# Kernel tuning notes

Hardware: AMD Instinct MI355X
Metric: run time of the kernel (lower is better)

Reference implementation:

```python
import jax, jax.numpy as jnp
import numpy as np

ALPHA = 1.702
LIMIT = 7.0
TOP_K = 4


def setup_inputs() -> dict:
    key = jax.random.key(0)
    ks = jax.random.split(key, 7)
    B, S, H, E, I = 2, 1024, 1024, 16, 2048
    scale_w = 1.0 / np.sqrt(H)
    return {
        "hidden_states": jax.random.normal(ks[0], (B, S, H), jnp.float32),
        "router_weight": jax.random.normal(ks[1], (E, H), jnp.float32) * scale_w,
        "router_bias": jax.random.normal(ks[2], (E,), jnp.float32) * 0.01,
        "gate_up_proj": jax.random.normal(ks[3], (E, H, 2 * I), jnp.float32) * scale_w,
        "gate_up_proj_bias": jax.random.normal(ks[4], (E, 2 * I), jnp.float32) * 0.01,
        "down_proj": jax.random.normal(ks[5], (E, I, H), jnp.float32) * (1.0 / np.sqrt(I)),
        "down_proj_bias": jax.random.normal(ks[6], (E, H), jnp.float32) * 0.01,
    }


def reference(hidden_states, router_weight, router_bias, gate_up_proj,
              gate_up_proj_bias, down_proj, down_proj_bias):
    B, S, H = hidden_states.shape
    E = router_weight.shape[0]
    dt = hidden_states.dtype

    # Router: linear -> softmax -> top-k -> renormalize
    router_logits = jnp.einsum('bsh,eh->bse', hidden_states, router_weight) + router_bias
    router_probs = jax.nn.softmax(router_logits, axis=-1)
    topk_weights, topk_indices = jax.lax.top_k(router_probs, TOP_K)  # [B,S,K]
    topk_weights = topk_weights / jnp.sum(topk_weights, axis=-1, keepdims=True)

    # Sparsity mask [B,S,E]: 1 for active experts (semantics of tt.sparse_matmul)
    onehot = jax.nn.one_hot(topk_indices, E, dtype=dt)        # [B,S,K,E]
    sparsity = jnp.sum(onehot, axis=2)                         # [B,S,E] (0/1)

    # Fused gate+up projection (interleaved layout), masked per-expert
    gate_up = jnp.einsum('bsh,ehf->bsef', hidden_states, gate_up_proj)  # [B,S,E,2I]
    gate_up = gate_up * sparsity[..., None]
    gate = gate_up[..., 0::2] + gate_up_proj_bias[:, 0::2]     # [B,S,E,I]
    up = gate_up[..., 1::2] + gate_up_proj_bias[:, 1::2]

    gate = jnp.minimum(gate, LIMIT)
    up = jnp.clip(up, -LIMIT, LIMIT)
    glu = gate * jax.nn.sigmoid(gate * ALPHA)
    activated = (up + 1.0) * glu                               # [B,S,E,I]

    # Down projection, masked per-expert, then bias
    down = jnp.einsum('bsei,eih->bseh', activated, down_proj)  # [B,S,E,H]
    down = down * sparsity[..., None] + down_proj_bias         # bias broadcasts [E,H]

    # Scatter top-k weights to full expert dim and combine
    full_weights = jnp.sum(onehot * topk_weights[..., None], axis=2)   # [B,S,E]
    output = jnp.sum(down * full_weights[..., None], axis=2)           # [B,S,H]
    return output, topk_weights
```

## Files before the change

kernel.cpp:

```cpp
#include <hip/hip_runtime.h>

#define TOKENS 2048
#define HD 1024
#define NEXP 16
#define TWO_I 4096
#define ID 2048

typedef short short8 __attribute__((ext_vector_type(8)));
typedef float f32x4 __attribute__((ext_vector_type(4)));
typedef unsigned short ushort;

static __device__ __forceinline__ ushort f2bf(float f) {
    union { float f; unsigned u; } v; v.f = f;
    unsigned r = v.u + 0x7FFFu + ((v.u >> 16) & 1u);
    return (ushort)(r >> 16);
}

static __device__ __forceinline__ void gload_lds16(const void* g, void* l) {
    __builtin_amdgcn_global_load_lds(
        (const __attribute__((address_space(1))) unsigned int*)(g),
        (__attribute__((address_space(3))) unsigned int*)(l), 16, 0, 0);
}

__global__ __launch_bounds__(256) void cvt_kernel(const float* __restrict__ hs,
                                                  ushort* __restrict__ hb) {
    int i = (blockIdx.x * 256 + threadIdx.x) * 4;
    float4 v = *(const float4*)(hs + i);
    union { ushort b[4]; float2 f2; } u;
    u.b[0] = f2bf(v.x); u.b[1] = f2bf(v.y); u.b[2] = f2bf(v.z); u.b[3] = f2bf(v.w);
    *(float2*)(hb + i) = u.f2;
}

__global__ __launch_bounds__(256) void transpose_cvt_kernel(
    const float* __restrict__ src, ushort* __restrict__ dst, int K, int N) {
    const int e = blockIdx.z;
    const int n0 = blockIdx.x * 64;
    const int k0 = blockIdx.y * 64;
    __shared__ float T[64][68];
    const float* s = src + (size_t)e * K * N + (size_t)k0 * N + n0;
    const int r = threadIdx.x >> 4;
    const int c4 = (threadIdx.x & 15) * 4;
#pragma unroll
    for (int i = 0; i < 64; i += 16) {
        float4 v = *(const float4*)(s + (size_t)(r + i) * N + c4);
        T[r + i][c4 + 0] = v.x; T[r + i][c4 + 1] = v.y;
        T[r + i][c4 + 2] = v.z; T[r + i][c4 + 3] = v.w;
    }
    __syncthreads();
    const int n = threadIdx.x >> 2;
    const int kc = (threadIdx.x & 3) * 16;
    union { ushort b[16]; short8 v[2]; } o;
#pragma unroll
    for (int j = 0; j < 16; ++j) o.b[j] = f2bf(T[kc + j][n]);
    ushort* d = dst + (size_t)e * N * K + (size_t)(n0 + n) * K + k0 + kc;
    *(short8*)(d) = o.v[0];
    *(short8*)(d + 8) = o.v[1];
}

__global__ __launch_bounds__(256) void router_kernel(
    const float* __restrict__ hs, const float* __restrict__ rw,
    const float* __restrict__ rb, float* __restrict__ topk_w_out,
    int* __restrict__ topk_idx, int* __restrict__ counts) {
    const int wave = threadIdx.x >> 6;
    const int lane = threadIdx.x & 63;
    const int t = blockIdx.x * 4 + wave;

    float h[16];
#pragma unroll
    for (int j = 0; j < 16; ++j) h[j] = hs[t * HD + j * 64 + lane];

    __shared__ float lg[4][NEXP];
#pragma unroll
    for (int e = 0; e < NEXP; ++e) {
        float acc = 0.f;
#pragma unroll
        for (int j = 0; j < 16; ++j) acc += h[j] * rw[e * HD + j * 64 + lane];
#pragma unroll
        for (int s = 32; s > 0; s >>= 1) acc += __shfl_xor(acc, s);
        if (lane == 0) lg[wave][e] = acc + rb[e];
    }
    if (lane == 0) {
        float mx = lg[wave][0];
        for (int e = 1; e < NEXP; ++e) mx = fmaxf(mx, lg[wave][e]);
        float pr[NEXP];
        for (int e = 0; e < NEXP; ++e) pr[e] = __expf(lg[wave][e] - mx);
        int idx[4]; float wv[4]; float sum4 = 0.f;
        for (int k = 0; k < 4; ++k) {
            int bi = 0; float bv = -1.f;
            for (int e = 0; e < NEXP; ++e)
                if (pr[e] > bv) { bv = pr[e]; bi = e; }
            idx[k] = bi; wv[k] = bv; pr[bi] = -2.f; sum4 += bv;
        }
        for (int k = 0; k < 4; ++k) {
            topk_w_out[t * 4 + k] = wv[k] / sum4;
            topk_idx[t * 4 + k] = idx[k];
            atomicAdd(&counts[idx[k]], 1);
        }
    }
}

__global__ void scan_kernel(const int* __restrict__ counts, int* __restrict__ offsets,
                            int* __restrict__ cursor) {
    if (threadIdx.x == 0 && blockIdx.x == 0) {
        int o = 0;
        for (int e = 0; e < NEXP; ++e) { offsets[e] = o; cursor[e] = o; o += counts[e]; }
        offsets[NEXP] = o;
    }
}

__global__ __launch_bounds__(256) void build_kernel(
    const int* __restrict__ topk_idx, const float* __restrict__ topk_w,
    int* __restrict__ cursor, int* __restrict__ token_list, float* __restrict__ slot_w) {
    int t = blockIdx.x * 256 + threadIdx.x;
    for (int k = 0; k < 4; ++k) {
        int e = topk_idx[t * 4 + k];
        int pos = atomicAdd(&cursor[e], 1);
        token_list[pos] = t;
        slot_w[pos] = topk_w[t * 4 + k];
    }
}


__global__ __launch_bounds__(256) void gemm1_t_kernel(
    const ushort* __restrict__ hb, const ushort* __restrict__ gupT,
    const float* __restrict__ gub, const int* __restrict__ offsets,
    const int* __restrict__ token_list, ushort* __restrict__ act) {
    const int e = blockIdx.z;
    const int so = offsets[e];
    const int ne = offsets[e + 1] - so;
    const int row0 = blockIdx.y * 128;
    if (row0 >= ne) return;
    const int n0 = blockIdx.x * 128;

    __shared__ ushort As[128 * 32];
    __shared__ ushort Bs[128 * 32];

    const int tid = threadIdx.x;
    const int lane = tid & 63;
    const int w = tid >> 6;
    const int m = lane & 15;
    const int q = lane >> 4;
    const int wm = (w >> 1) * 64;
    const int wn = (w & 1) * 64;

    const int r0 = tid >> 2;
    const int ce = (tid & 3) * 8;
    int ar0 = row0 + r0;       if (ar0 >= ne) ar0 = ne - 1;
    int ar1 = row0 + 64 + r0;  if (ar1 >= ne) ar1 = ne - 1;
    const ushort* ga0 = hb + (size_t)token_list[so + ar0] * HD + ce;
    const ushort* ga1 = hb + (size_t)token_list[so + ar1] * HD + ce;
    const ushort* gb0 = gupT + (size_t)e * TWO_I * HD + (size_t)(n0 + r0) * HD + ce;
    const ushort* gb1 = gb0 + (size_t)64 * HD;
    ushort* lA0 = As + w * 512;
    ushort* lA1 = As + 2048 + w * 512;
    ushort* lB0 = Bs + w * 512;
    ushort* lB1 = Bs + 2048 + w * 512;

    f32x4 acc[4][4] = {};

    for (int k0 = 0; k0 < HD; k0 += 32) {
        gload_lds16(ga0 + k0, lA0);
        gload_lds16(ga1 + k0, lA1);
        gload_lds16(gb0 + k0, lB0);
        gload_lds16(gb1 + k0, lB1);
        asm volatile("s_waitcnt vmcnt(0)" ::: "memory");
        __syncthreads();
        short8 af[4], bf[4];
#pragma unroll
        for (int rt = 0; rt < 4; ++rt)
            af[rt] = *(const short8*)(As + (wm + rt * 16 + m) * 32 + q * 8);
#pragma unroll
        for (int c = 0; c < 4; ++c)
            bf[c] = *(const short8*)(Bs + (wn + c * 16 + m) * 32 + q * 8);
#pragma unroll
        for (int rt = 0; rt < 4; ++rt)
#pragma unroll
            for (int c = 0; c < 4; ++c)
                acc[rt][c] = __builtin_amdgcn_mfma_f32_16x16x32_bf16(af[rt], bf[c], acc[rt][c], 0, 0, 0);
        __syncthreads();
    }

#pragma unroll
    for (int c = 0; c < 4; ++c) {
        const int n = n0 + wn + c * 16 + m;
        const float bias = gub[e * TWO_I + n];
#pragma unroll
        for (int rt = 0; rt < 4; ++rt) {
#pragma unroll
            for (int rr = 0; rr < 4; ++rr) {
                const int grow = row0 + wm + rt * 16 + q * 4 + rr;
                float v = acc[rt][c][rr] + bias;
                float pv = __shfl_xor(v, 1);
                float gate = (m & 1) ? pv : v;
                float up   = (m & 1) ? v : pv;
                gate = fminf(gate, 7.0f);
                up = fminf(fmaxf(up, -7.0f), 7.0f);
                float glu = gate / (1.0f + __expf(-1.702f * gate));
                float a = (up + 1.0f) * glu;
                if (!(m & 1) && grow < ne)
                    act[(size_t)(so + grow) * ID + (n >> 1)] = f2bf(a);
            }
        }
    }
}

__global__ __launch_bounds__(256) void gemm2_t_kernel(
    const ushort* __restrict__ act, const ushort* __restrict__ downT,
    const float* __restrict__ dwb, const int* __restrict__ offsets,
    const int* __restrict__ token_list, const float* __restrict__ slot_w,
    float* __restrict__ out) {
    const int e = blockIdx.z;
    const int so = offsets[e];
    const int ne = offsets[e + 1] - so;
    const int row0 = blockIdx.y * 128;
    if (row0 >= ne) return;
    const int n0 = blockIdx.x * 128;

    __shared__ ushort As[128 * 32];
    __shared__ ushort Bs[128 * 32];

    const int tid = threadIdx.x;
    const int lane = tid & 63;
    const int w = tid >> 6;
    const int m = lane & 15;
    const int q = lane >> 4;
    const int wm = (w >> 1) * 64;
    const int wn = (w & 1) * 64;

    const int r0 = tid >> 2;
    const int ce = (tid & 3) * 8;
    const ushort* ga0 = act + (size_t)(so + row0 + r0) * ID + ce;
    const ushort* ga1 = ga0 + (size_t)64 * ID;
    const ushort* gb0 = downT + (size_t)e * HD * ID + (size_t)(n0 + r0) * ID + ce;
    const ushort* gb1 = gb0 + (size_t)64 * ID;
    ushort* lA0 = As + w * 512;
    ushort* lA1 = As + 2048 + w * 512;
    ushort* lB0 = Bs + w * 512;
    ushort* lB1 = Bs + 2048 + w * 512;

    f32x4 acc[4][4] = {};

    for (int k0 = 0; k0 < ID; k0 += 32) {
        gload_lds16(ga0 + k0, lA0);
        gload_lds16(ga1 + k0, lA1);
        gload_lds16(gb0 + k0, lB0);
        gload_lds16(gb1 + k0, lB1);
        asm volatile("s_waitcnt vmcnt(0)" ::: "memory");
        __syncthreads();
        short8 af[4], bf[4];
#pragma unroll
        for (int rt = 0; rt < 4; ++rt)
            af[rt] = *(const short8*)(As + (wm + rt * 16 + m) * 32 + q * 8);
#pragma unroll
        for (int c = 0; c < 4; ++c)
            bf[c] = *(const short8*)(Bs + (wn + c * 16 + m) * 32 + q * 8);
#pragma unroll
        for (int rt = 0; rt < 4; ++rt)
#pragma unroll
            for (int c = 0; c < 4; ++c)
                acc[rt][c] = __builtin_amdgcn_mfma_f32_16x16x32_bf16(af[rt], bf[c], acc[rt][c], 0, 0, 0);
        __syncthreads();
    }

    float bias[4];
#pragma unroll
    for (int c = 0; c < 4; ++c) bias[c] = dwb[e * HD + n0 + wn + c * 16 + m];

#pragma unroll
    for (int rt = 0; rt < 4; ++rt) {
#pragma unroll
        for (int rr = 0; rr < 4; ++rr) {
            const int grow = row0 + wm + rt * 16 + q * 4 + rr;
            if (grow < ne) {
                const int slot = so + grow;
                const int tok = token_list[slot];
                const float wgt = slot_w[slot];
#pragma unroll
                for (int c = 0; c < 4; ++c) {
                    const int n = n0 + wn + c * 16 + m;
                    atomicAdd(&out[tok * HD + n], (acc[rt][c][rr] + bias[c]) * wgt);
                }
            }
        }
    }
}


__global__ __launch_bounds__(256) void gemm1_fb_kernel(
    const ushort* __restrict__ hb, const float* __restrict__ gup,
    const float* __restrict__ gub, const int* __restrict__ offsets,
    const int* __restrict__ token_list, ushort* __restrict__ act) {
    const int e = blockIdx.z;
    const int so = offsets[e];
    const int ne = offsets[e + 1] - so;
    const int row0 = blockIdx.y * 64;
    if (row0 >= ne) return;
    const int n0 = blockIdx.x * 64;
    __shared__ ushort Al[64][40];
    __shared__ ushort Bt[64][40];
    const int tid = threadIdx.x;
    const int lane = tid & 63;
    const int wave = tid >> 6;
    const int m = lane & 15;
    const int q = lane >> 4;
    const int ar = tid >> 2;
    const int ac = (tid & 3) * 8;
    int arow = row0 + ar; if (arow >= ne) arow = ne - 1;
    const int tok = token_list[so + arow];
    const ushort* aptr = hb + tok * HD + ac;
    const int bk = tid >> 3;
    const int bn = (tid & 7) * 8;
    const float* bptr = gup + (size_t)e * HD * TWO_I + (size_t)bk * TWO_I + n0 + bn;
    f32x4 acc[4] = {{0,0,0,0},{0,0,0,0},{0,0,0,0},{0,0,0,0}};
    for (int k0 = 0; k0 < HD; k0 += 32) {
        float4 av = *(const float4*)(aptr + k0);
        *(float4*)(&Al[ar][ac]) = av;
        const float* bp = bptr + (size_t)k0 * TWO_I;
        float4 b0 = *(const float4*)(bp);
        float4 b1 = *(const float4*)(bp + 4);
        Bt[bn + 0][bk] = f2bf(b0.x); Bt[bn + 1][bk] = f2bf(b0.y);
        Bt[bn + 2][bk] = f2bf(b0.z); Bt[bn + 3][bk] = f2bf(b0.w);
        Bt[bn + 4][bk] = f2bf(b1.x); Bt[bn + 5][bk] = f2bf(b1.y);
        Bt[bn + 6][bk] = f2bf(b1.z); Bt[bn + 7][bk] = f2bf(b1.w);
        __syncthreads();
        short8 af = *(const short8*)(&Al[wave * 16 + m][q * 8]);
#pragma unroll
        for (int c = 0; c < 4; ++c) {
            short8 bf = *(const short8*)(&Bt[c * 16 + m][q * 8]);
            acc[c] = __builtin_amdgcn_mfma_f32_16x16x32_bf16(af, bf, acc[c], 0, 0, 0);
        }
        __syncthreads();
    }
#pragma unroll
    for (int c = 0; c < 4; ++c) {
        const int n = n0 + c * 16 + m;
        const float bias = gub[e * TWO_I + n];
#pragma unroll
        for (int r = 0; r < 4; ++r) {
            const int grow = row0 + wave * 16 + q * 4 + r;
            float v = acc[c][r] + bias;
            float pv = __shfl_xor(v, 1);
            float gate = (m & 1) ? pv : v;
            float up   = (m & 1) ? v : pv;
            gate = fminf(gate, 7.0f);
            up = fminf(fmaxf(up, -7.0f), 7.0f);
            float glu = gate / (1.0f + __expf(-1.702f * gate));
            float a = (up + 1.0f) * glu;
            if (!(m & 1) && grow < ne)
                act[(size_t)(so + grow) * ID + (n >> 1)] = f2bf(a);
        }
    }
}

__global__ __launch_bounds__(256) void gemm2_fb_kernel(
    const ushort* __restrict__ act, const float* __restrict__ dwp,
    const float* __restrict__ dwb, const int* __restrict__ offsets,
    const int* __restrict__ token_list, const float* __restrict__ slot_w,
    float* __restrict__ out) {
    const int e = blockIdx.z;
    const int so = offsets[e];
    const int ne = offsets[e + 1] - so;
    const int row0 = blockIdx.y * 64;
    if (row0 >= ne) return;
    const int n0 = blockIdx.x * 64;
    __shared__ ushort Al[64][40];
    __shared__ ushort Bt[64][40];
    const int tid = threadIdx.x;
    const int lane = tid & 63;
    const int wave = tid >> 6;
    const int m = lane & 15;
    const int q = lane >> 4;
    const int ar = tid >> 2;
    const int ac = (tid & 3) * 8;
    int arow = row0 + ar; if (arow >= ne) arow = ne - 1;
    const ushort* aptr = act + (size_t)(so + arow) * ID + ac;
    const int bk = tid >> 3;
    const int bn = (tid & 7) * 8;
    const float* bptr = dwp + (size_t)e * ID * HD + (size_t)bk * HD + n0 + bn;
    f32x4 acc[4] = {{0,0,0,0},{0,0,0,0},{0,0,0,0},{0,0,0,0}};
    for (int k0 = 0; k0 < ID; k0 += 32) {
        float4 av = *(const float4*)(aptr + k0);
        *(float4*)(&Al[ar][ac]) = av;
        const float* bp = bptr + (size_t)k0 * HD;
        float4 b0 = *(const float4*)(bp);
        float4 b1 = *(const float4*)(bp + 4);
        Bt[bn + 0][bk] = f2bf(b0.x); Bt[bn + 1][bk] = f2bf(b0.y);
        Bt[bn + 2][bk] = f2bf(b0.z); Bt[bn + 3][bk] = f2bf(b0.w);
        Bt[bn + 4][bk] = f2bf(b1.x); Bt[bn + 5][bk] = f2bf(b1.y);
        Bt[bn + 6][bk] = f2bf(b1.z); Bt[bn + 7][bk] = f2bf(b1.w);
        __syncthreads();
        short8 af = *(const short8*)(&Al[wave * 16 + m][q * 8]);
#pragma unroll
        for (int c = 0; c < 4; ++c) {
            short8 bf = *(const short8*)(&Bt[c * 16 + m][q * 8]);
            acc[c] = __builtin_amdgcn_mfma_f32_16x16x32_bf16(af, bf, acc[c], 0, 0, 0);
        }
        __syncthreads();
    }
#pragma unroll
    for (int r = 0; r < 4; ++r) {
        const int grow = row0 + wave * 16 + q * 4 + r;
        if (grow < ne) {
            const int slot = so + grow;
            const int tok = token_list[slot];
            const float wgt = slot_w[slot];
#pragma unroll
            for (int c = 0; c < 4; ++c) {
                const int n = n0 + c * 16 + m;
                atomicAdd(&out[tok * HD + n], (acc[c][r] + dwb[e * HD + n]) * wgt);
            }
        }
    }
}

extern "C" void kernel_launch(void* const* d_in, const int* in_sizes, int n_in,
                              void* d_out, int out_size, void* d_ws, size_t ws_size,
                              hipStream_t stream) {
    const float* hs  = (const float*)d_in[0];
    const float* rw  = (const float*)d_in[1];
    const float* rb  = (const float*)d_in[2];
    const float* gup = (const float*)d_in[3];
    const float* gub = (const float*)d_in[4];
    const float* dwp = (const float*)d_in[5];
    const float* dwb = (const float*)d_in[6];

    float* out = (float*)d_out;
    float* topk_w = out + (size_t)TOKENS * HD;

    char* w = (char*)d_ws;
    int* counts     = (int*)(w + 0);
    int* cursor     = (int*)(w + 64);
    int* offsets    = (int*)(w + 128);
    int* token_list = (int*)(w + 256);
    float* slot_w   = (float*)(w + 256 + 32768);
    int* topk_idx   = (int*)(w + 256 + 65536);
    ushort* hb      = (ushort*)(w + (1 << 20));
    ushort* act     = (ushort*)(w + (size_t)(6 << 20));
    ushort* gupT    = (ushort*)(w + (size_t)(41 << 20));
    ushort* downT   = (ushort*)(w + (size_t)(169 << 20));
    const size_t need = (size_t)(233) << 20;

    hipMemsetAsync(w, 0, 256, stream);
    hipMemsetAsync(out, 0, (size_t)TOKENS * HD * sizeof(float), stream);

    cvt_kernel<<<2048, 256, 0, stream>>>(hs, hb);
    router_kernel<<<512, 256, 0, stream>>>(hs, rw, rb, topk_w, topk_idx, counts);
    scan_kernel<<<1, 64, 0, stream>>>(counts, offsets, cursor);
    build_kernel<<<8, 256, 0, stream>>>(topk_idx, topk_w, cursor, token_list, slot_w);

    if (ws_size >= need) {
        transpose_cvt_kernel<<<dim3(TWO_I / 64, HD / 64, NEXP), 256, 0, stream>>>(
            gup, gupT, HD, TWO_I);
        transpose_cvt_kernel<<<dim3(HD / 64, ID / 64, NEXP), 256, 0, stream>>>(
            dwp, downT, ID, HD);
        gemm1_t_kernel<<<dim3(TWO_I / 128, TOKENS / 128, NEXP), 256, 0, stream>>>(
            hb, gupT, gub, offsets, token_list, act);
        gemm2_t_kernel<<<dim3(HD / 128, TOKENS / 128, NEXP), 256, 0, stream>>>(
            act, downT, dwb, offsets, token_list, slot_w, out);
    } else {
        gemm1_fb_kernel<<<dim3(TWO_I / 64, TOKENS / 64, NEXP), 256, 0, stream>>>(
            hb, gup, gub, offsets, token_list, act);
        gemm2_fb_kernel<<<dim3(HD / 64, TOKENS / 64, NEXP), 256, 0, stream>>>(
            act, dwp, dwb, offsets, token_list, slot_w, out);
    }
}
```

Before: 818.5 us.

## Replace atomic scatter in down-projection with per-slot buffer and combine kernel

The down-projection GEMM now writes unweighted per-slot results to a dense partial buffer instead of doing float atomicAdds into the output. A new combine kernel gathers each token's four slots through a slot map built in the routing step and writes the weighted sum directly, which also removes the output memset on the fast path. The transpose LDS tile padding changes from 68 to 65 columns to reduce bank conflicts. The cost is an extra 32 MB buffer, an additional kernel launch and more workspace.

Measured after the change: 820.2 us. No clear change (+0.2%).

```diff
diff --git a/kernel.cpp b/kernel.cpp
--- a/kernel.cpp
+++ b/kernel.cpp
@@ -36,7 +36,7 @@
     const int e = blockIdx.z;
     const int n0 = blockIdx.x * 64;
     const int k0 = blockIdx.y * 64;
-    __shared__ float T[64][68];
+    __shared__ float T[64][65];
     const float* s = src + (size_t)e * K * N + (size_t)k0 * N + n0;
     const int r = threadIdx.x >> 4;
     const int c4 = (threadIdx.x & 15) * 4;
@@ -110,16 +110,17 @@
 
 __global__ __launch_bounds__(256) void build_kernel(
     const int* __restrict__ topk_idx, const float* __restrict__ topk_w,
-    int* __restrict__ cursor, int* __restrict__ token_list, float* __restrict__ slot_w) {
+    int* __restrict__ cursor, int* __restrict__ token_list, float* __restrict__ slot_w,
+    int* __restrict__ slot_map) {
     int t = blockIdx.x * 256 + threadIdx.x;
     for (int k = 0; k < 4; ++k) {
         int e = topk_idx[t * 4 + k];
         int pos = atomicAdd(&cursor[e], 1);
         token_list[pos] = t;
         slot_w[pos] = topk_w[t * 4 + k];
-    }
-}
-
+        slot_map[t * 4 + k] = pos;
+    }
+}
 
 __global__ __launch_bounds__(256) void gemm1_t_kernel(
     const ushort* __restrict__ hb, const ushort* __restrict__ gupT,
@@ -207,8 +208,7 @@
 __global__ __launch_bounds__(256) void gemm2_t_kernel(
     const ushort* __restrict__ act, const ushort* __restrict__ downT,
     const float* __restrict__ dwb, const int* __restrict__ offsets,
-    const int* __restrict__ token_list, const float* __restrict__ slot_w,
-    float* __restrict__ out) {
+    float* __restrict__ part) {
     const int e = blockIdx.z;
     const int so = offsets[e];
     const int ne = offsets[e + 1] - so;
@@ -272,17 +272,30 @@
         for (int rr = 0; rr < 4; ++rr) {
             const int grow = row0 + wm + rt * 16 + q * 4 + rr;
             if (grow < ne) {
-                const int slot = so + grow;
-                const int tok = token_list[slot];
-                const float wgt = slot_w[slot];
-#pragma unroll
-                for (int c = 0; c < 4; ++c) {
-                    const int n = n0 + wn + c * 16 + m;
-                    atomicAdd(&out[tok * HD + n], (acc[rt][c][rr] + bias[c]) * wgt);
-                }
+                float* p = part + (size_t)(so + grow) * HD;
+#pragma unroll
+                for (int c = 0; c < 4; ++c)
+                    p[n0 + wn + c * 16 + m] = acc[rt][c][rr] + bias[c];
             }
         }
     }
+}
+
+__global__ __launch_bounds__(256) void combine_kernel(
+    const float* __restrict__ part, const int* __restrict__ slot_map,
+    const float* __restrict__ slot_w, float* __restrict__ out) {
+    const int t = blockIdx.x;
+    const int h = threadIdx.x * 4;
+    float4 acc = {0.f, 0.f, 0.f, 0.f};
+#pragma unroll
+    for (int k = 0; k < 4; ++k) {
+        const int s = slot_map[t * 4 + k];
+        const float wk = slot_w[s];
+        float4 v = *(const float4*)(part + (size_t)s * HD + h);
+        acc.x += wk * v.x; acc.y += wk * v.y;
+        acc.z += wk * v.z; acc.w += wk * v.w;
+    }
+    *(float4*)(out + (size_t)t * HD + h) = acc;
 }
 
 
@@ -434,19 +447,21 @@
     int* token_list = (int*)(w + 256);
     float* slot_w   = (float*)(w + 256 + 32768);
     int* topk_idx   = (int*)(w + 256 + 65536);
+    int* slot_map   = (int*)(w + 256 + 98304);
     ushort* hb      = (ushort*)(w + (1 << 20));
     ushort* act     = (ushort*)(w + (size_t)(6 << 20));
     ushort* gupT    = (ushort*)(w + (size_t)(41 << 20));
     ushort* downT   = (ushort*)(w + (size_t)(169 << 20));
-    const size_t need = (size_t)(233) << 20;
+    float*  part    = (float*)(w + (size_t)(240 << 20));
+    const size_t need = (size_t)(272) << 20;
 
     hipMemsetAsync(w, 0, 256, stream);
-    hipMemsetAsync(out, 0, (size_t)TOKENS * HD * sizeof(float), stream);
 
     cvt_kernel<<<2048, 256, 0, stream>>>(hs, hb);
     router_kernel<<<512, 256, 0, stream>>>(hs, rw, rb, topk_w, topk_idx, counts);
     scan_kernel<<<1, 64, 0, stream>>>(counts, offsets, cursor);
-    build_kernel<<<8, 256, 0, stream>>>(topk_idx, topk_w, cursor, token_list, slot_w);
+    build_kernel<<<8, 256, 0, stream>>>(topk_idx, topk_w, cursor, token_list, slot_w,
+                                        slot_map);
 
     if (ws_size >= need) {
         transpose_cvt_kernel<<<dim3(TWO_I / 64, HD / 64, NEXP), 256, 0, stream>>>(
@@ -456,8 +471,10 @@
         gemm1_t_kernel<<<dim3(TWO_I / 128, TOKENS / 128, NEXP), 256, 0, stream>>>(
             hb, gupT, gub, offsets, token_list, act);
         gemm2_t_kernel<<<dim3(HD / 128, TOKENS / 128, NEXP), 256, 0, stream>>>(
-            act, downT, dwb, offsets, token_list, slot_w, out);
+            act, downT, dwb, offsets, part);
+        combine_kernel<<<TOKENS, 256, 0, stream>>>(part, slot_map, slot_w, out);
     } else {
+        hipMemsetAsync(out, 0, (size_t)TOKENS * HD * sizeof(float), stream);
         gemm1_fb_kernel<<<dim3(TWO_I / 64, TOKENS / 64, NEXP), 256, 0, stream>>>(
             hb, gup, gub, offsets, token_list, act);
         gemm2_fb_kernel<<<dim3(HD / 64, TOKENS / 64, NEXP), 256, 0, stream>>>(
```
